# Optimization experiments

Measured on AMD Instinct MI355X. Metric: run time of the kernel, lower is better.

The kernel has to match this reference:

```python
import jax, jax.numpy as jnp
import numpy as np


def _bce_with_logits(x, t):
    # numerically-stable binary_cross_entropy_with_logits, reduction='none'
    return jnp.maximum(x, 0.0) - x * t + jnp.log1p(jnp.exp(-jnp.abs(x)))


def _compute_weights(targets):
    """Replicates the scipy.ndimage.label / sum_labels weighting.

    4-connected component labeling (scipy default structure) via iterative
    min-label propagation, then per-pixel component area, then
    1 / (sqrt(area) + 1) with zeros replaced by the global mean of the
    nonzero sqrt-areas.
    """
    B, H, W = targets.shape
    HW = H * W  # sentinel label for background
    fg = targets > 0
    base = jnp.arange(HW, dtype=jnp.int32).reshape(1, H, W)
    lab0 = jnp.where(fg, base, HW).astype(jnp.int32)

    def cond(state):
        return state[1]

    def body(state):
        lab, _ = state
        p = jnp.pad(lab, ((0, 0), (1, 1), (1, 1)), constant_values=HW)
        nb = jnp.minimum(jnp.minimum(p[:, :-2, 1:-1], p[:, 2:, 1:-1]),
                         jnp.minimum(p[:, 1:-1, :-2], p[:, 1:-1, 2:]))
        new = jnp.where(fg, jnp.minimum(lab, nb), HW)
        return new, jnp.any(new != lab)

    lab, _ = jax.lax.while_loop(cond, body, (lab0, jnp.array(True)))

    def per_sample_area(lab_i, fg_i):
        sizes = jax.ops.segment_sum(fg_i.ravel().astype(jnp.float32),
                                    lab_i.ravel(), num_segments=HW + 1)
        return sizes[lab_i]  # [H, W] area of each pixel's component

    area = jax.vmap(per_sample_area)(lab, fg)
    area = jnp.where(fg, area, 0.0)

    w = jnp.sqrt(area)
    nz = w > 0
    # global (whole-tensor) mean of nonzero sqrt-areas, as in the torch code
    mean_nz = jnp.sum(jnp.where(nz, w, 0.0)) / jnp.maximum(
        jnp.sum(nz.astype(jnp.float32)), 1.0)
    w_filled = jnp.where(nz, w, mean_nz)
    return 1.0 / (w_filled + 1.0)


def setup_inputs() -> dict:
    key = jax.random.key(0)
    k1, k2 = jax.random.split(key)
    B, H, W = 32, 512, 512
    inputs = jax.random.normal(k1, (B, H, W), dtype=jnp.float32)
    # sparse binary mask (subcritical density -> small blobs, like vessels)
    targets = (jax.random.uniform(k2, (B, H, W)) < 0.3).astype(jnp.float32)
    return {"inputs": inputs, "targets": targets}


def reference(inputs, targets):
    weights = _compute_weights(targets)
    bce = _bce_with_logits(inputs, targets)
    return jnp.mean(weights * bce)
```

## Files before the change

kernel.cpp:

```cpp
#include <hip/hip_runtime.h>
#include <math.h>

static constexpr int IMG_W  = 512;
static constexpr int IMG_PX = 512 * 512;
static constexpr int NIMG   = 32;
static constexpr int TILE_W = 64;
static constexpr int TILE_H = 32;
static constexpr int TPX    = IMG_W / TILE_W;
static constexpr int TPY    = IMG_W / TILE_H;
static constexpr int TILES_PER_IMG = TPX * TPY;
static constexpr int FUSED_BLOCKS  = NIMG * TILES_PER_IMG;
static constexpr int ECAP_T  = 48;
static constexpr int SCAP    = 128;
static constexpr int NE      = TILES_PER_IMG * ECAP_T;
static constexpr int NSS     = TILES_PER_IMG * SCAP;
static constexpr int FLAGBIT = 1 << 30;
static constexpr int CNT12   = 0xFFF;
static constexpr int SLOTSH  = 12;
static constexpr int TPIX    = TILE_W * TILE_H;


__device__ __forceinline__ void cstore_d(double* p, double v) {
    __hip_atomic_store(p, v, __ATOMIC_RELAXED, __HIP_MEMORY_SCOPE_AGENT);
}
__device__ __forceinline__ double cload_d(const double* p) {
    return __hip_atomic_load((double*)p, __ATOMIC_RELAXED, __HIP_MEMORY_SCOPE_AGENT);
}


__device__ __forceinline__ int find_root_l(volatile int* sl, int x) {
    int p = sl[x];
    while (p != x) { x = p; p = sl[x]; }
    return p;
}

__device__ __forceinline__ void merge_l(int* sl, int a, int b) {
    while (true) {
        a = find_root_l(sl, a);
        b = find_root_l(sl, b);
        if (a == b) return;
        if (a < b) { int t = a; a = b; b = t; }
        int old = atomicMin(&sl[a], b);
        if (old == a) return;
        a = old;
    }
}

__device__ __forceinline__ void block_reduce_write(float s_fg, float s_bg,
                                                   float s_sq, float s_n,
                                                   double4* __restrict__ part,
                                                   int slot) {
    for (int o = 32; o > 0; o >>= 1) {
        s_fg += __shfl_down(s_fg, o, 64);
        s_bg += __shfl_down(s_bg, o, 64);
        s_sq += __shfl_down(s_sq, o, 64);
        s_n  += __shfl_down(s_n,  o, 64);
    }
    __shared__ double4 wsum[4];
    int wave = threadIdx.x >> 6;
    if ((threadIdx.x & 63) == 0)
        wsum[wave] = make_double4((double)s_fg, (double)s_bg, (double)s_sq, (double)s_n);
    __syncthreads();
    if (threadIdx.x == 0) {
        double4 b = wsum[0];
        for (int wv = 1; wv < 4; wv++) {
            b.x += wsum[wv].x; b.y += wsum[wv].y;
            b.z += wsum[wv].z; b.w += wsum[wv].w;
        }
        part[slot] = b;
    }
}

__device__ __forceinline__ float bce0_fast(float xx) {
    return fmaxf(xx, 0.f) + __logf(1.f + __expf(-fabsf(xx)));
}


__global__ __launch_bounds__(256, 8) void ccl_fused(const float* __restrict__ t,
                                                    const float* __restrict__ x,
                                                    int* __restrict__ L,
                                                    int2* __restrict__ ilist,
                                                    int* __restrict__ blockcount,
                                                    int2* __restrict__ seams,
                                                    int* __restrict__ seamcount,
                                                    double4* __restrict__ part) {
    __shared__ int   sl[TPIX];
    __shared__ int   cnt[TPIX];
    __shared__ float fsumS[64];
    __shared__ unsigned long long rowmask[TILE_H];
    __shared__ int   lcount, scount;

    int blk = blockIdx.x;
    int b   = blk / TILES_PER_IMG;
    int tid = blk % TILES_PER_IMG;
    int tY  = tid / TPX, tX = tid % TPX;
    int k   = threadIdx.x;
    int col = k & 63, wv = k >> 6;
    int base = b * IMG_PX + (tY * TILE_H) * IMG_W + tX * TILE_W;

    if (k == 0) { lcount = 0; scount = 0; }
    if (k < 64) fsumS[k] = 0.f;

    float xr[8];
    unsigned int fgbits = 0;
#pragma unroll
    for (int s = 0; s < 8; s++) {
        int row = wv * 8 + s;
        int jj  = row * TILE_W + col;
        int g   = base + row * IMG_W + col;
        float tv = t[g];
        xr[s] = x[g];
        bool fg = (tv != 0.f);
        fgbits |= (unsigned)fg << s;
        unsigned long long mask = __ballot(fg);
        if (col == 0) rowmask[row] = mask;
        int lab = jj;
        if (fg) {
            unsigned long long startm = mask & ~(mask << 1);
            unsigned long long low = (col == 63) ? ~0ULL : ((1ULL << (col + 1)) - 1ULL);
            lab = row * TILE_W + (63 - __clzll(startm & low));
        }
        sl[jj]  = lab;
        cnt[jj] = 0;
    }
    __syncthreads();

#pragma unroll
    for (int s = 0; s < 8; s++) {
        int row = wv * 8 + s;
        if (row == 0) continue;
        unsigned long long both = rowmask[row] & rowmask[row - 1];
        unsigned long long pairstart = both & ~(both << 1);
        if ((pairstart >> col) & 1ULL)
            merge_l(sl, row * TILE_W + col, (row - 1) * TILE_W + col);
    }
    __syncthreads();

#pragma unroll
    for (int s = 0; s < 8; s++) {
        int row = wv * 8 + s;
        unsigned long long mask = rowmask[row];
        unsigned long long startm = mask & ~(mask << 1);
        if ((startm >> col) & 1ULL) {
            unsigned long long inv = ~(mask >> col);
            int len = inv ? (__ffsll((long long)inv) - 1) : (64 - col);
            int jj = row * TILE_W + col;
            int r = find_root_l(sl, jj);
            sl[jj] = r;
            atomicAdd(&cnt[r], len);
        }
    }
    __syncthreads();

    {
        int r = -1, c = 0, dg = 0; bool owner = false;
        if      (k < 64)  { r = 0;          c = k;        dg = (tY > 0)       ? -IMG_W : 0; }
        else if (k < 128) { r = TILE_H - 1; c = k - 64;   dg = (tY < TPY - 1) ?  IMG_W : 0; owner = true; }
        else if (k < 160) { r = k - 128;    c = 0;        dg = (tX > 0)       ? -1     : 0; }
        else if (k < 192) { r = k - 160;    c = TILE_W-1; dg = (tX < TPX - 1) ?  1     : 0; owner = true; }
        if (r >= 0) {
            int g = base + r * IMG_W + c;
            bool fg = (rowmask[r] >> c) & 1ULL;
            if (fg) {
                int jj = r * TILE_W + c;
                int root = sl[sl[jj]];
                L[g] = base + (root >> 6) * IMG_W + (root & 63);
                if (dg != 0 && t[g + dg] != 0.f) {
                    int old = atomicOr(&cnt[root], FLAGBIT);
                    if (!(old & FLAGBIT)) {
                        int slot = min(atomicAdd(&lcount, 1), 63);
                        atomicOr(&cnt[root], slot << SLOTSH);
                    }
                    if (owner) {
                        int s = atomicAdd(&scount, 1);
                        if (s < SCAP) seams[blk * SCAP + s] = make_int2(g, g + dg);
                    }
                }
            }
        }
    }
    __syncthreads();

    float s_fg = 0.f, s_bg = 0.f, s_sq = 0.f, s_n = 0.f;
#pragma unroll
    for (int s = 0; s < 8; s++) {
        int row = wv * 8 + s;
        int jj  = row * TILE_W + col;
        float xx = xr[s];
        float b0 = bce0_fast(xx);
        int s0   = sl[jj];
        int root = sl[s0];
        int cc   = cnt[root];
        bool fg  = (fgbits >> s) & 1u;
        float bce1 = b0 - xx;
        if (cc & FLAGBIT) {
            atomicAdd(&fsumS[(cc >> SLOTSH) & 63], bce1);
        } else {
            float w   = sqrtf((float)cc);
            float inv = 1.f / (w + 1.f);
            s_fg += fg ? bce1 * inv : 0.f;
            s_bg += fg ? 0.f : b0;
            s_sq += w;
            s_n  += fg ? 1.f : 0.f;
        }
    }
    __syncthreads();

#pragma unroll
    for (int s = 0; s < 8; s++) {
        int jj = (wv * 8 + s) * TILE_W + col;
        if (sl[jj] == jj) {
            int cj = cnt[jj];
            if (cj & FLAGBIT) {
                int slot = (cj >> SLOTSH) & 63;
                if (slot < ECAP_T) {
                    ilist[blk * ECAP_T + slot] =
                        make_int2(__float_as_int(fsumS[slot]), cj & CNT12);
                    int g = base + (jj >> 6) * IMG_W + (jj & 63);
                    L[g] = -(tid * ECAP_T + slot) - 2;
                }
            }
        }
    }
    block_reduce_write(s_fg, s_bg, s_sq, s_n, part, blk);
    if (k == 0) { blockcount[blk] = min(lcount, ECAP_T); seamcount[blk] = min(scount, SCAP); }
}


__global__ __launch_bounds__(1024) void tail(const int* __restrict__ L,
                                             const int2* __restrict__ ilist,
                                             const int* __restrict__ blockcount,
                                             const int2* __restrict__ seams,
                                             const int* __restrict__ seamcount,
                                             const double4* __restrict__ part,
                                             double* __restrict__ imgAcc,
                                             int* __restrict__ done,
                                             float* __restrict__ out,
                                             int N) {
    __shared__ int parent[NE];
    __shared__ int areaL[NE];
    __shared__ int sc[TILES_PER_IMG];
    __shared__ int bc[TILES_PER_IMG];
    __shared__ double4 wsum[16];
    __shared__ int elect_r;

    int b = blockIdx.x, k = threadIdx.x;
    int tb = b * TILES_PER_IMG;
    const int2* mySeams = seams + (size_t)tb * SCAP;
    const int2* myIlist = ilist + (size_t)tb * ECAP_T;

    if (k < TILES_PER_IMG) {
        sc[k] = min(seamcount[tb + k], SCAP);
        bc[k] = min(blockcount[tb + k], ECAP_T);
    }
    for (int i = k; i < NE; i += 1024) { parent[i] = i; areaL[i] = 0; }
    __syncthreads();

    for (int b0 = 0; b0 < NSS; b0 += 1024 * 4) {
        int va[4], vb[4];
#pragma unroll
        for (int j = 0; j < 4; j++) {
            int i = b0 + j * 1024 + k;
            int tile = i >> 7, slot = i & (SCAP - 1);
            bool valid = slot < sc[tile];
            int2 pr = valid ? mySeams[i] : make_int2(-1, -1);
            va[j] = pr.x; vb[j] = pr.y;
        }
#pragma unroll
        for (int j = 0; j < 4; j++) {
            if (va[j] >= 0) va[j] = L[va[j]];
            if (vb[j] >= 0) vb[j] = L[vb[j]];
        }
#pragma unroll
        for (int j = 0; j < 4; j++) {
            if (va[j] >= 0) va[j] = L[va[j]];
            if (vb[j] >= 0) vb[j] = L[vb[j]];
        }
#pragma unroll
        for (int j = 0; j < 4; j++) {
            int e1 = -va[j] - 2, e2 = -vb[j] - 2;
            if (e1 >= 0 && e1 < NE && e2 >= 0 && e2 < NE)
                merge_l(parent, e1, e2);
        }
    }
    __syncthreads();

    for (int b0 = 0; b0 < NE; b0 += 1024 * 4) {
        int ct[4], rt[4];
#pragma unroll
        for (int j = 0; j < 4; j++) {
            int i = b0 + j * 1024 + k;
            ct[j] = 0;
            if (i < NE) {
                int tile = i / ECAP_T, slot = i - tile * ECAP_T;
                if (slot < bc[tile]) ct[j] = myIlist[i].y;
            }
        }
#pragma unroll
        for (int j = 0; j < 4; j++) {
            int i = b0 + j * 1024 + k;
            rt[j] = 0;
            if (i < NE) { rt[j] = find_root_l(parent, i); parent[i] = rt[j]; }
        }
#pragma unroll
        for (int j = 0; j < 4; j++)
            if (ct[j] > 0) atomicAdd(&areaL[rt[j]], ct[j]);
    }
    __syncthreads();

    float t_fg = 0.f, t_sq = 0.f, t_n = 0.f;
    for (int b0 = 0; b0 < NE; b0 += 1024 * 4) {
        int fb[4], ct[4];
#pragma unroll
        for (int j = 0; j < 4; j++) {
            int i = b0 + j * 1024 + k;
            fb[j] = 0; ct[j] = 0;
            if (i < NE) {
                int tile = i / ECAP_T, slot = i - tile * ECAP_T;
                if (slot < bc[tile]) {
                    int2 e = myIlist[i]; fb[j] = e.x; ct[j] = e.y;
                }
            }
        }
#pragma unroll
        for (int j = 0; j < 4; j++) {
            if (ct[j] > 0) {
                int i = b0 + j * 1024 + k;
                float w = sqrtf((float)areaL[parent[i]]);
                t_fg += __int_as_float(fb[j]) / (w + 1.f);
                t_sq += (float)ct[j] * w;
                t_n  += (float)ct[j];
            }
        }
    }

    double fg = (double)t_fg, bg = 0.0, sq = (double)t_sq, nn = (double)t_n;
    if (k < TILES_PER_IMG) {
        double4 p = part[tb + k];
        fg += p.x; bg += p.y; sq += p.z; nn += p.w;
    }
    for (int o = 32; o > 0; o >>= 1) {
        fg += __shfl_down(fg, o, 64);
        bg += __shfl_down(bg, o, 64);
        sq += __shfl_down(sq, o, 64);
        nn += __shfl_down(nn, o, 64);
    }
    if ((k & 63) == 0) wsum[k >> 6] = make_double4(fg, bg, sq, nn);
    __syncthreads();
    if (k == 0) {
        double4 bb = wsum[0];
        for (int w2 = 1; w2 < 16; w2++) {
            bb.x += wsum[w2].x; bb.y += wsum[w2].y;
            bb.z += wsum[w2].z; bb.w += wsum[w2].w;
        }
        cstore_d(&imgAcc[b * 4 + 0], bb.x);
        cstore_d(&imgAcc[b * 4 + 1], bb.y);
        cstore_d(&imgAcc[b * 4 + 2], bb.z);
        cstore_d(&imgAcc[b * 4 + 3], bb.w);
    }

    __syncthreads();
    if (k == 0) elect_r = atomicAdd(done, 1);
    __syncthreads();
    if (elect_r != NIMG - 1) return;

    double tfg = 0.0, tbg = 0.0, tsq = 0.0, tnn = 0.0;
    if (k < NIMG) {
        tfg = cload_d(&imgAcc[k * 4 + 0]);
        tbg = cload_d(&imgAcc[k * 4 + 1]);
        tsq = cload_d(&imgAcc[k * 4 + 2]);
        tnn = cload_d(&imgAcc[k * 4 + 3]);
    }
    if (k < 64) {
        for (int o = 32; o > 0; o >>= 1) {
            tfg += __shfl_down(tfg, o, 64);
            tbg += __shfl_down(tbg, o, 64);
            tsq += __shfl_down(tsq, o, 64);
            tnn += __shfl_down(tnn, o, 64);
        }
        if (k == 0) {
            double mean_nz = tsq / fmax(tnn, 1.0);
            double loss = (tfg + tbg / (mean_nz + 1.0)) / (double)N;
            out[0] = (float)loss;
        }
    }
}


extern "C" void kernel_launch(void* const* d_in, const int* in_sizes, int n_in,
                              void* d_out, int out_size, void* d_ws, size_t ws_size,
                              hipStream_t stream) {
    const float* x = (const float*)d_in[0];
    const float* t = (const float*)d_in[1];
    float* out = (float*)d_out;
    int N = in_sizes[0];

    int* L          = (int*)d_ws;
    int* blockcount = L + N;
    int* seamcount  = blockcount + FUSED_BLOCKS;
    int* done       = seamcount + FUSED_BLOCKS;
    double4* part   = (double4*)(done + 8);
    double* imgAcc  = (double*)(part + FUSED_BLOCKS);
    int2* ilist     = (int2*)(imgAcc + NIMG * 4);
    int2* seams     = ilist + (size_t)FUSED_BLOCKS * ECAP_T;

    hipMemsetAsync(done, 0, 8 * sizeof(int), stream);

    ccl_fused<<<FUSED_BLOCKS, 256, 0, stream>>>(t, x, L, ilist, blockcount,
                                                seams, seamcount, part);
    tail<<<NIMG, 1024, 0, stream>>>(L, ilist, blockcount, seams, seamcount,
                                    part, imgAcc, done, out, N);
}
```

Measured before the change: 152.1 us.

## Enlarge CCL tiles to 64x64 with 512 threads and fold done-reset into kernel

Doubles the tile height so each fused block labels a 64x64 tile with 512 threads. This halves the number of tiles per image, so fewer seam pairs and cross-tile entries are left for the tail union-find. The slot and count bit fields are widened to match, and the reduction is inlined for 8 waves. The separate memset of the done counter is replaced by a write from block 0 inside the fused kernel, which saves one launch. In exchange, shared memory per block doubles, which can lower occupancy, and the done reset now depends on ordering between the two kernels.

Measured after the change: 143.4 us. -5.7%, faster.

```diff
diff --git a/kernel.cpp b/kernel.cpp
--- a/kernel.cpp
+++ b/kernel.cpp
@@ -5,18 +5,19 @@
 static constexpr int IMG_PX = 512 * 512;
 static constexpr int NIMG   = 32;
 static constexpr int TILE_W = 64;
-static constexpr int TILE_H = 32;
+static constexpr int TILE_H = 64;
 static constexpr int TPX    = IMG_W / TILE_W;
 static constexpr int TPY    = IMG_W / TILE_H;
 static constexpr int TILES_PER_IMG = TPX * TPY;
 static constexpr int FUSED_BLOCKS  = NIMG * TILES_PER_IMG;
-static constexpr int ECAP_T  = 48;
+static constexpr int ECAP_T  = 96;
 static constexpr int SCAP    = 128;
 static constexpr int NE      = TILES_PER_IMG * ECAP_T;
 static constexpr int NSS     = TILES_PER_IMG * SCAP;
+static constexpr int CNT13   = 0x1FFF;
+static constexpr int SLOTSH  = 13;
+static constexpr int SLOTMK  = 127;
 static constexpr int FLAGBIT = 1 << 30;
-static constexpr int CNT12   = 0xFFF;
-static constexpr int SLOTSH  = 12;
 static constexpr int TPIX    = TILE_W * TILE_H;
 
 
@@ -46,49 +47,26 @@
     }
 }
 
-__device__ __forceinline__ void block_reduce_write(float s_fg, float s_bg,
-                                                   float s_sq, float s_n,
-                                                   double4* __restrict__ part,
-                                                   int slot) {
-    for (int o = 32; o > 0; o >>= 1) {
-        s_fg += __shfl_down(s_fg, o, 64);
-        s_bg += __shfl_down(s_bg, o, 64);
-        s_sq += __shfl_down(s_sq, o, 64);
-        s_n  += __shfl_down(s_n,  o, 64);
-    }
-    __shared__ double4 wsum[4];
-    int wave = threadIdx.x >> 6;
-    if ((threadIdx.x & 63) == 0)
-        wsum[wave] = make_double4((double)s_fg, (double)s_bg, (double)s_sq, (double)s_n);
-    __syncthreads();
-    if (threadIdx.x == 0) {
-        double4 b = wsum[0];
-        for (int wv = 1; wv < 4; wv++) {
-            b.x += wsum[wv].x; b.y += wsum[wv].y;
-            b.z += wsum[wv].z; b.w += wsum[wv].w;
-        }
-        part[slot] = b;
-    }
-}
-
 __device__ __forceinline__ float bce0_fast(float xx) {
     return fmaxf(xx, 0.f) + __logf(1.f + __expf(-fabsf(xx)));
 }
 
 
-__global__ __launch_bounds__(256, 8) void ccl_fused(const float* __restrict__ t,
+__global__ __launch_bounds__(512, 8) void ccl_fused(const float* __restrict__ t,
                                                     const float* __restrict__ x,
                                                     int* __restrict__ L,
                                                     int2* __restrict__ ilist,
                                                     int* __restrict__ blockcount,
                                                     int2* __restrict__ seams,
                                                     int* __restrict__ seamcount,
-                                                    double4* __restrict__ part) {
+                                                    double4* __restrict__ part,
+                                                    int* __restrict__ done) {
     __shared__ int   sl[TPIX];
     __shared__ int   cnt[TPIX];
-    __shared__ float fsumS[64];
+    __shared__ float fsumS[128];
     __shared__ unsigned long long rowmask[TILE_H];
     __shared__ int   lcount, scount;
+    __shared__ double4 wsum[8];
 
     int blk = blockIdx.x;
     int b   = blk / TILES_PER_IMG;
@@ -99,10 +77,12 @@
     int base = b * IMG_PX + (tY * TILE_H) * IMG_W + tX * TILE_W;
 
     if (k == 0) { lcount = 0; scount = 0; }
-    if (k < 64) fsumS[k] = 0.f;
+    if (k < 128) fsumS[k] = 0.f;
+    if (blk == 0 && k == 0) *done = 0;
 
     float xr[8];
     unsigned int fgbits = 0;
+    unsigned long long low = (col == 63) ? ~0ULL : ((1ULL << (col + 1)) - 1ULL);
 #pragma unroll
     for (int s = 0; s < 8; s++) {
         int row = wv * 8 + s;
@@ -117,7 +97,6 @@
         int lab = jj;
         if (fg) {
             unsigned long long startm = mask & ~(mask << 1);
-            unsigned long long low = (col == 63) ? ~0ULL : ((1ULL << (col + 1)) - 1ULL);
             lab = row * TILE_W + (63 - __clzll(startm & low));
         }
         sl[jj]  = lab;
@@ -156,8 +135,8 @@
         int r = -1, c = 0, dg = 0; bool owner = false;
         if      (k < 64)  { r = 0;          c = k;        dg = (tY > 0)       ? -IMG_W : 0; }
         else if (k < 128) { r = TILE_H - 1; c = k - 64;   dg = (tY < TPY - 1) ?  IMG_W : 0; owner = true; }
-        else if (k < 160) { r = k - 128;    c = 0;        dg = (tX > 0)       ? -1     : 0; }
-        else if (k < 192) { r = k - 160;    c = TILE_W-1; dg = (tX < TPX - 1) ?  1     : 0; owner = true; }
+        else if (k < 192) { r = k - 128;    c = 0;        dg = (tX > 0)       ? -1     : 0; }
+        else if (k < 256) { r = k - 192;    c = TILE_W-1; dg = (tX < TPX - 1) ?  1     : 0; owner = true; }
         if (r >= 0) {
             int g = base + r * IMG_W + c;
             bool fg = (rowmask[r] >> c) & 1ULL;
@@ -168,7 +147,7 @@
                 if (dg != 0 && t[g + dg] != 0.f) {
                     int old = atomicOr(&cnt[root], FLAGBIT);
                     if (!(old & FLAGBIT)) {
-                        int slot = min(atomicAdd(&lcount, 1), 63);
+                        int slot = min(atomicAdd(&lcount, 1), SLOTMK);
                         atomicOr(&cnt[root], slot << SLOTSH);
                     }
                     if (owner) {
@@ -194,7 +173,7 @@
         bool fg  = (fgbits >> s) & 1u;
         float bce1 = b0 - xx;
         if (cc & FLAGBIT) {
-            atomicAdd(&fsumS[(cc >> SLOTSH) & 63], bce1);
+            atomicAdd(&fsumS[(cc >> SLOTSH) & SLOTMK], bce1);
         } else {
             float w   = sqrtf((float)cc);
             float inv = 1.f / (w + 1.f);
@@ -212,18 +191,37 @@
         if (sl[jj] == jj) {
             int cj = cnt[jj];
             if (cj & FLAGBIT) {
-                int slot = (cj >> SLOTSH) & 63;
+                int slot = (cj >> SLOTSH) & SLOTMK;
                 if (slot < ECAP_T) {
                     ilist[blk * ECAP_T + slot] =
-                        make_int2(__float_as_int(fsumS[slot]), cj & CNT12);
+                        make_int2(__float_as_int(fsumS[slot]), cj & CNT13);
                     int g = base + (jj >> 6) * IMG_W + (jj & 63);
                     L[g] = -(tid * ECAP_T + slot) - 2;
                 }
             }
         }
     }
-    block_reduce_write(s_fg, s_bg, s_sq, s_n, part, blk);
-    if (k == 0) { blockcount[blk] = min(lcount, ECAP_T); seamcount[blk] = min(scount, SCAP); }
+
+    for (int o = 32; o > 0; o >>= 1) {
+        s_fg += __shfl_down(s_fg, o, 64);
+        s_bg += __shfl_down(s_bg, o, 64);
+        s_sq += __shfl_down(s_sq, o, 64);
+        s_n  += __shfl_down(s_n,  o, 64);
+    }
+    if ((k & 63) == 0)
+        wsum[wv] = make_double4((double)s_fg, (double)s_bg,
+                                (double)s_sq, (double)s_n);
+    __syncthreads();
+    if (k == 0) {
+        double4 bb = wsum[0];
+        for (int w2 = 1; w2 < 8; w2++) {
+            bb.x += wsum[w2].x; bb.y += wsum[w2].y;
+            bb.z += wsum[w2].z; bb.w += wsum[w2].w;
+        }
+        part[blk] = bb;
+        blockcount[blk] = min(lcount, ECAP_T);
+        seamcount[blk]  = min(scount, SCAP);
+    }
 }
 
 
@@ -262,7 +260,7 @@
         for (int j = 0; j < 4; j++) {
             int i = b0 + j * 1024 + k;
             int tile = i >> 7, slot = i & (SCAP - 1);
-            bool valid = slot < sc[tile];
+            bool valid = (i < NSS) && (slot < sc[tile]);
             int2 pr = valid ? mySeams[i] : make_int2(-1, -1);
             va[j] = pr.x; vb[j] = pr.y;
         }
@@ -404,10 +402,9 @@
     int2* ilist     = (int2*)(imgAcc + NIMG * 4);
     int2* seams     = ilist + (size_t)FUSED_BLOCKS * ECAP_T;
 
-    hipMemsetAsync(done, 0, 8 * sizeof(int), stream);
-
-    ccl_fused<<<FUSED_BLOCKS, 256, 0, stream>>>(t, x, L, ilist, blockcount,
-                                                seams, seamcount, part);
+
+    ccl_fused<<<FUSED_BLOCKS, 512, 0, stream>>>(t, x, L, ilist, blockcount,
+                                                seams, seamcount, part, done);
     tail<<<NIMG, 1024, 0, stream>>>(L, ilist, blockcount, seams, seamcount,
                                     part, imgAcc, done, out, N);
 }
```
